# Kernel optimization log

Measured on AMD Instinct MI355X. Metric: run time of the kernel, lower is better.

Reference implementation:

```python
import jax, jax.numpy as jnp
import numpy as np

D = 768; H = 12; T = 8; E = 4; L = 197; B = 4; BT = B * T


def _ln(x, g, b):
    m = x.mean(-1, keepdims=True)
    v = ((x - m) ** 2).mean(-1, keepdims=True)
    return (x - m) / jnp.sqrt(v + 1e-5) * g + b


def _qgelu(x):
    return x * jax.nn.sigmoid(1.702 * x)


def _mha(x, wqkv, bqkv, wo, bo):
    # x: (L, N, D), torch nn.MultiheadAttention semantics (seq-first)
    Lx, N, Dm = x.shape
    hd = Dm // H
    qkv = x @ wqkv.T + bqkv                      # (L, N, 3D)
    q, k, v = jnp.split(qkv, 3, axis=-1)
    sh = lambda t: t.reshape(Lx, N, H, hd).transpose(1, 2, 0, 3)  # (N,H,L,hd)
    q, k, v = sh(q), sh(k), sh(v)
    att = jax.nn.softmax(jnp.einsum('nhld,nhmd->nhlm', q, k) / np.sqrt(hd).astype(np.float32), -1)
    o = jnp.einsum('nhlm,nhmd->nhld', att, v).transpose(2, 0, 1, 3).reshape(Lx, N, Dm)
    return o @ wo.T + bo


def setup_inputs() -> dict:
    key = jax.random.key(0)
    ks = iter(jax.random.split(key, 40))
    s = 0.02
    p = {}
    p['x'] = jax.random.normal(next(ks), (L, BT, D), jnp.float32)
    p['msg_fc_w'] = s * jax.random.normal(next(ks), (D, D)); p['msg_fc_b'] = jnp.zeros((D,))
    p['msg_ln_g'] = jnp.ones((D,)); p['msg_ln_b'] = jnp.zeros((D,))
    p['msg_attn_wqkv'] = s * jax.random.normal(next(ks), (3 * D, D)); p['msg_attn_bqkv'] = jnp.zeros((3 * D,))
    p['msg_attn_wo'] = s * jax.random.normal(next(ks), (D, D)); p['msg_attn_bo'] = jnp.zeros((D,))
    p['attn_wqkv'] = s * jax.random.normal(next(ks), (3 * D, D)); p['attn_bqkv'] = jnp.zeros((3 * D,))
    p['attn_wo'] = s * jax.random.normal(next(ks), (D, D)); p['attn_bo'] = jnp.zeros((D,))
    p['ln1_g'] = jnp.ones((D,)); p['ln1_b'] = jnp.zeros((D,))
    p['ln2_g'] = jnp.ones((D,)); p['ln2_b'] = jnp.zeros((D,))
    p['cfc_w'] = s * jax.random.normal(next(ks), (4 * D, D)); p['cfc_b'] = jnp.zeros((4 * D,))
    p['cproj_w'] = s * jax.random.normal(next(ks), (D, 4 * D)); p['cproj_b'] = jnp.zeros((D,))
    p['eh_w'] = s * jax.random.normal(next(ks), (E, 4 * D, D)); p['eh_b'] = jnp.zeros((E, 4 * D))
    p['et_w'] = s * jax.random.normal(next(ks), (E, D, 4 * D)); p['et_b'] = jnp.zeros((E, D))
    p['r1_w'] = s * jax.random.normal(next(ks), (E + 1, D)); p['r1_b'] = jnp.zeros((E + 1,))
    p['r2_w'] = s * jax.random.normal(next(ks), (E + 1, 4 * D)); p['r2_b'] = jnp.zeros((E + 1,))
    return p


def reference(x, msg_fc_w, msg_fc_b, msg_ln_g, msg_ln_b, msg_attn_wqkv, msg_attn_bqkv,
              msg_attn_wo, msg_attn_bo, attn_wqkv, attn_bqkv, attn_wo, attn_bo,
              ln1_g, ln1_b, ln2_g, ln2_b, cfc_w, cfc_b, cproj_w, cproj_b,
              eh_w, eh_b, et_w, et_b, r1_w, r1_b, r2_w, r2_b):
    l, bt, d = x.shape
    b = bt // T
    x4 = x.reshape(l, b, T, d)
    # message token from CLS (position 0) of each frame
    msg = x4[0] @ msg_fc_w.T + msg_fc_b          # (b, T, d)
    msg = msg.transpose(1, 0, 2)                 # (T, b, d) - attend across frames
    mln = _ln(msg, msg_ln_g, msg_ln_b)
    msg = msg + _mha(mln, msg_attn_wqkv, msg_attn_bqkv, msg_attn_wo, msg_attn_bo)
    msg_r = msg.transpose(1, 0, 2)[None]         # (1, b, T, d)
    xc = jnp.concatenate([x4, msg_r], axis=0).reshape(l + 1, bt, d)
    xc = xc + _mha(_ln(xc, ln1_g, ln1_b), attn_wqkv, attn_bqkv, attn_wo, attn_bo)
    x = xc[:l]
    ln_x = _ln(x, ln2_g, ln2_b)
    # soft-MoE head: shared c_fc is expert 0, then E expert heads
    Wh = jnp.concatenate([cfc_w[None], eh_w], 0)     # (E+1, 4D, D)
    bh = jnp.concatenate([cfc_b[None], eh_b], 0)     # (E+1, 4D)
    heads = jnp.einsum('lbd,efd->lbef', ln_x, Wh) + bh  # (l, bt, E+1, 4D)
    r1 = jax.nn.softmax(ln_x @ r1_w.T + r1_b, -1)       # (l, bt, E+1)
    oh = jnp.einsum('lbe,lbef->lbf', r1, heads)
    oh = _qgelu(oh)
    # soft-MoE tail
    Wt = jnp.concatenate([cproj_w[None], et_w], 0)   # (E+1, D, 4D)
    btl = jnp.concatenate([cproj_b[None], et_b], 0)  # (E+1, D)
    tails = jnp.einsum('lbf,edf->lbed', oh, Wt) + btl  # (l, bt, E+1, D)
    r2 = jax.nn.softmax(oh @ r2_w.T + r2_b, -1)
    out = jnp.einsum('lbe,lbed->lbd', r2, tails)
    return x + out
```

## Files before the change

kernel.cpp:

```cpp
#include <hip/hip_runtime.h>
#include <hip/hip_bf16.h>

typedef __hip_bfloat16 bf16;
typedef __attribute__((ext_vector_type(8))) short short8;
typedef __attribute__((ext_vector_type(4))) float f32x4;

__device__ __forceinline__ float b2f(bf16 v){ return __bfloat162float(v); }
__device__ __forceinline__ unsigned short f2bits(float v){
  bf16 h = __float2bfloat16(v);
  return *reinterpret_cast<unsigned short*>(&h);
}

__device__ __forceinline__ void gload16(const bf16* g, bf16* l){
  __builtin_amdgcn_global_load_lds((const __attribute__((address_space(1))) void*)g,
                                   (__attribute__((address_space(3))) void*)l, 16, 0, 0);
}

__device__ __forceinline__ void ld4(const float* p, float& a,float& b,float& c,float& d){
  float4 v = *reinterpret_cast<const float4*>(p); a=v.x; b=v.y; c=v.z; d=v.w;
}
__device__ __forceinline__ float wave_sum(float v){
  #pragma unroll
  for (int off=32; off>0; off>>=1) v += __shfl_down(v, off);
  return v;
}

__device__ __forceinline__ int xcd_swz(int wg, int nwg){
  int q = nwg >> 3, r = nwg & 7;
  int x = wg & 7, i = wg >> 3;
  return (x < r ? x*(q+1) : r*(q+1) + (x-r)*q) + i;
}

__global__ __launch_bounds__(256) void prep_weights(
    const float* __restrict__ s0, const float* __restrict__ s1,
    const float* __restrict__ s2, const float* __restrict__ s3,
    const float* __restrict__ s4, const float* __restrict__ s5,
    bf16* __restrict__ d0, bf16* __restrict__ d1, bf16* __restrict__ d2,
    bf16* __restrict__ d3, bf16* __restrict__ d4, bf16* __restrict__ d5){
  long i4 = (long)blockIdx.x*256 + threadIdx.x;
  const float* s; bf16* d; long base;
  if      (i4 <  442368){ s=s0; d=d0; base=0; }
  else if (i4 <  589824){ s=s1; d=d1; base=442368; }
  else if (i4 < 1179648){ s=s2; d=d2; base=589824; }
  else if (i4 < 3538944){ s=s3; d=d3; base=1179648; }
  else if (i4 < 4128768){ s=s4; d=d4; base=3538944; }
  else                  { s=s5; d=d5; base=4128768; }
  long j = (i4 - base)*4;
  float4 v = *reinterpret_cast<const float4*>(s + j);
  d[j]   = __float2bfloat16(v.x);
  d[j+1] = __float2bfloat16(v.y);
  d[j+2] = __float2bfloat16(v.z);
  d[j+3] = __float2bfloat16(v.w);
}

__global__ __launch_bounds__(256) void prep_bias(
    const float* __restrict__ cfc_b, const float* __restrict__ eh_b,
    const float* __restrict__ cproj_b, const float* __restrict__ et_b,
    float* __restrict__ bias_h, float* __restrict__ bias_t){
  int i = blockIdx.x*256 + threadIdx.x;
  if (i < 3072)       bias_h[i] = cfc_b[i];
  else if (i < 15360) bias_h[i] = eh_b[i-3072];
  else if (i < 16128) bias_t[i-15360] = cproj_b[i-15360];
  else if (i < 19200) bias_t[i-15360] = et_b[i-16128];
}

__global__ __launch_bounds__(256) void ln_rows(const float* __restrict__ in,
    const float* __restrict__ g, const float* __restrict__ b,
    float* __restrict__ out){
  int row = blockIdx.x;
  const float* x = in + (size_t)row*768;
  float* o = out + (size_t)row*768;
  float s=0.f, s2=0.f;
  for (int d=threadIdx.x; d<768; d+=256){ float v=x[d]; s+=v; s2+=v*v; }
  s = wave_sum(s); s2 = wave_sum(s2);
  __shared__ float red[8];
  __shared__ float stat[2];
  int lane = threadIdx.x & 63, wid = threadIdx.x >> 6;
  if (lane==0){ red[wid]=s; red[4+wid]=s2; }
  __syncthreads();
  if (threadIdx.x==0){
    float S=red[0]+red[1]+red[2]+red[3];
    float S2=red[4]+red[5]+red[6]+red[7];
    float m = S*(1.f/768.f);
    float var = S2*(1.f/768.f) - m*m;
    stat[0]=m; stat[1]=rsqrtf(var + 1e-5f);
  }
  __syncthreads();
  float m=stat[0], inv=stat[1];
  for (int d=threadIdx.x; d<768; d+=256)
    o[d] = (x[d]-m)*inv*g[d] + b[d];
}

__global__ __launch_bounds__(256) void ln_rows_b(const float* __restrict__ in,
    const float* __restrict__ g, const float* __restrict__ b,
    bf16* __restrict__ out){
  int row = blockIdx.x;
  const float* x = in + (size_t)row*768;
  bf16* o = out + (size_t)row*768;
  float s=0.f, s2=0.f;
  for (int d=threadIdx.x; d<768; d+=256){ float v=x[d]; s+=v; s2+=v*v; }
  s = wave_sum(s); s2 = wave_sum(s2);
  __shared__ float red[8];
  __shared__ float stat[2];
  int lane = threadIdx.x & 63, wid = threadIdx.x >> 6;
  if (lane==0){ red[wid]=s; red[4+wid]=s2; }
  __syncthreads();
  if (threadIdx.x==0){
    float S=red[0]+red[1]+red[2]+red[3];
    float S2=red[4]+red[5]+red[6]+red[7];
    float m = S*(1.f/768.f);
    float var = S2*(1.f/768.f) - m*m;
    stat[0]=m; stat[1]=rsqrtf(var + 1e-5f);
  }
  __syncthreads();
  float m=stat[0], inv=stat[1];
  for (int d=threadIdx.x; d<768; d+=256)
    o[d] = __float2bfloat16((x[d]-m)*inv*g[d] + b[d]);
}

template<int K>
__global__ __launch_bounds__(256) void router2(const bf16* __restrict__ X,
    const float* __restrict__ W, const float* __restrict__ bias,
    float* __restrict__ out, int rows){
  int row = blockIdx.x*4 + (threadIdx.x>>6);
  int lane = threadIdx.x & 63;
  if (row >= rows) return;
  const bf16* x = X + (size_t)row*K;
  constexpr int NC = K/64;
  float xa[NC];
  #pragma unroll
  for (int c=0;c<NC;++c) xa[c] = b2f(x[c*64 + lane]);
  float lg[5];
  #pragma unroll
  for (int e=0;e<5;++e){
    const float* w = W + (size_t)e*K;
    float p=0.f;
    #pragma unroll
    for (int c=0;c<NC;++c) p += xa[c]*w[c*64 + lane];
    lg[e] = wave_sum(p);
  }
  if (lane==0){
    float mx=-1e30f;
    #pragma unroll
    for (int e=0;e<5;++e){ lg[e] += bias[e]; mx = fmaxf(mx, lg[e]); }
    float s=0.f;
    #pragma unroll
    for (int e=0;e<5;++e){ lg[e]=expf(lg[e]-mx); s+=lg[e]; }
    float inv=1.f/s;
    #pragma unroll
    for (int e=0;e<5;++e) out[(size_t)row*5+e] = lg[e]*inv;
  }
}

__global__ __launch_bounds__(64) void msg_attn(const float* __restrict__ mqkv,
    float* __restrict__ mattno){
  int bh = blockIdx.x; int b = bh/12, h = bh%12;
  __shared__ float qs[8][64], ks[8][64], vs[8][64], sc[8][8];
  int lane = threadIdx.x;
  for (int i=lane; i<512; i+=64){
    int t=i>>6, d=i&63;
    size_t base = ((size_t)(b*8+t))*2304 + h*64 + d;
    qs[t][d]=mqkv[base]; ks[t][d]=mqkv[base+768]; vs[t][d]=mqkv[base+1536];
  }
  __syncthreads();
  { int t=lane>>3, m=lane&7; float a=0.f;
    #pragma unroll
    for (int d=0;d<64;++d) a += qs[t][d]*ks[m][d];
    sc[t][m] = a*0.125f; }
  __syncthreads();
  if (lane<8){
    int t=lane; float mx=-1e30f;
    #pragma unroll
    for (int m=0;m<8;++m) mx=fmaxf(mx, sc[t][m]);
    float s=0.f;
    #pragma unroll
    for (int m=0;m<8;++m){ float e=expf(sc[t][m]-mx); sc[t][m]=e; s+=e; }
    float inv=1.f/s;
    #pragma unroll
    for (int m=0;m<8;++m) sc[t][m]*=inv;
  }
  __syncthreads();
  { int t=lane>>3, d0=(lane&7)*8;
    for (int dd=0; dd<8; ++dd){
      int d=d0+dd; float a=0.f;
      #pragma unroll
      for (int m=0;m<8;++m) a += sc[t][m]*vs[m][d];
      mattno[((size_t)(b*8+t))*768 + h*64 + d] = a;
    } }
}

__global__ __launch_bounds__(256) void attn_mfma(const bf16* __restrict__ qkv,
    bf16* __restrict__ attno){
  constexpr int KP = 232;
  __shared__ __align__(16) unsigned short Ks[208*72];
  __shared__ __align__(16) unsigned short Vt[64*KP];
  __shared__ __align__(16) unsigned short Ps[4*16*KP];

  int tid = threadIdx.x;
  int bh = blockIdx.x; int bb = bh/12, h = bh%12;
  int l0 = blockIdx.y*64;
  int wv = tid>>6, ln = tid&63, quad = ln>>4, mrow = ln&15;

  for (int i=tid; i<1584; i+=256){
    int m=i>>3, dc=(i&7)<<3;
    const uint4 kv = *reinterpret_cast<const uint4*>(qkv + ((size_t)(m*32+bb))*2304 + 768 + h*64 + dc);
    *reinterpret_cast<uint4*>(Ks + m*72 + dc) = kv;
    const uint4 vv = *reinterpret_cast<const uint4*>(qkv + ((size_t)(m*32+bb))*2304 + 1536 + h*64 + dc);
    unsigned int w[4] = {vv.x, vv.y, vv.z, vv.w};
    #pragma unroll
    for (int j=0;j<4;++j){
      Vt[(dc+2*j  )*KP + m] = (unsigned short)(w[j] & 0xffff);
      Vt[(dc+2*j+1)*KP + m] = (unsigned short)(w[j] >> 16);
    }
  }
  for (int i=tid; i<10*72; i+=256) Ks[198*72 + i] = 0;
  for (int i=tid; i<64*34; i+=256){ int d=i/34, c=198+(i%34); Vt[d*KP+c] = 0; }
  { unsigned int* pz = reinterpret_cast<unsigned int*>(Ps);
    for (int i=tid; i<4*16*KP/2; i+=256) pz[i] = 0; }

  int ql = l0 + wv*16 + mrow;
  short8 aq[2] = { {0,0,0,0,0,0,0,0}, {0,0,0,0,0,0,0,0} };
  if (ql < 198){
    aq[0] = *reinterpret_cast<const short8*>(qkv + ((size_t)(ql*32+bb))*2304 + h*64 + quad*8);
    aq[1] = *reinterpret_cast<const short8*>(qkv + ((size_t)(ql*32+bb))*2304 + h*64 + 32 + quad*8);
  }
  __syncthreads();

  f32x4 sc[13];
  const f32x4 zero = {0.f,0.f,0.f,0.f};
  #pragma unroll
  for (int t=0;t<13;++t){
    const short8 bk0 = *reinterpret_cast<const short8*>(Ks + (t*16+mrow)*72 + quad*8);
    const short8 bk1 = *reinterpret_cast<const short8*>(Ks + (t*16+mrow)*72 + 32 + quad*8);
    f32x4 a = zero;
    a = __builtin_amdgcn_mfma_f32_16x16x32_bf16(aq[0], bk0, a, 0,0,0);
    a = __builtin_amdgcn_mfma_f32_16x16x32_bf16(aq[1], bk1, a, 0,0,0);
    sc[t] = a * 0.125f;
  }
  if (192 + mrow >= 198) sc[12] = (f32x4){-1e30f,-1e30f,-1e30f,-1e30f};

  float inv[4];
  #pragma unroll
  for (int r=0;r<4;++r){
    float m = -1e30f;
    #pragma unroll
    for (int t=0;t<13;++t) m = fmaxf(m, sc[t][r]);
    #pragma unroll
    for (int msk=1; msk<16; msk<<=1) m = fmaxf(m, __shfl_xor(m, msk));
    float s = 0.f;
    #pragma unroll
    for (int t=0;t<13;++t){ float e = __expf(sc[t][r]-m); sc[t][r]=e; s+=e; }
    #pragma unroll
    for (int msk=1; msk<16; msk<<=1) s += __shfl_xor(s, msk);
    inv[r] = 1.f/s;
  }

  #pragma unroll
  for (int t=0;t<13;++t)
    #pragma unroll
    for (int r=0;r<4;++r)
      Ps[(wv*16 + quad*4+r)*KP + t*16+mrow] = f2bits(sc[t][r]);
  __syncthreads();

  f32x4 o[4] = {zero,zero,zero,zero};
  #pragma unroll
  for (int kc=0;kc<7;++kc){
    const short8 ap = *reinterpret_cast<const short8*>(Ps + (wv*16+mrow)*KP + kc*32 + quad*8);
    #pragma unroll
    for (int nt=0;nt<4;++nt){
      const short8 bv = *reinterpret_cast<const short8*>(Vt + (nt*16+mrow)*KP + kc*32 + quad*8);
      o[nt] = __builtin_amdgcn_mfma_f32_16x16x32_bf16(ap, bv, o[nt], 0,0,0);
    }
  }
  #pragma unroll
  for (int r=0;r<4;++r){
    int l = l0 + wv*16 + quad*4 + r;
    if (l >= 198) continue;
    #pragma unroll
    for (int nt=0;nt<4;++nt){
      int d = nt*16 + mrow;
      attno[((size_t)(l*32+bb))*768 + h*64 + d] = __float2bfloat16(o[nt][r]*inv[r]);
    }
  }
}

__global__ __launch_bounds__(256) void gemm_nt(const float* __restrict__ A,
    const float* __restrict__ B, const float* __restrict__ bias,
    const float* res, float* C,
    int M, int N, int K){
  __shared__ __align__(16) float As[16][68];
  __shared__ __align__(16) float Bs[16][68];
  int tid=threadIdx.x, tx=tid&15, ty=tid>>4;
  int row0=blockIdx.y*64, col0=blockIdx.x*64;
  int lrow=tid>>2, lk4=(tid&3)*4;
  float acc[4][4]={};
  for (int kb=0; kb<K; kb+=16){
    int gr = row0 + lrow;
    if (gr < M){
      float a0,a1,a2,a3; ld4(A + (size_t)gr*K + kb + lk4, a0,a1,a2,a3);
      As[lk4][lrow]=a0; As[lk4+1][lrow]=a1; As[lk4+2][lrow]=a2; As[lk4+3][lrow]=a3;
    } else {
      As[lk4][lrow]=0.f; As[lk4+1][lrow]=0.f; As[lk4+2][lrow]=0.f; As[lk4+3][lrow]=0.f;
    }
    { float c0,c1,c2,c3; ld4(B + (size_t)(col0+lrow)*K + kb + lk4, c0,c1,c2,c3);
      Bs[lk4][lrow]=c0; Bs[lk4+1][lrow]=c1; Bs[lk4+2][lrow]=c2; Bs[lk4+3][lrow]=c3; }
    __syncthreads();
    #pragma unroll
    for (int kk=0;kk<16;++kk){
      float4 a4 = *reinterpret_cast<const float4*>(&As[kk][ty*4]);
      float4 b4 = *reinterpret_cast<const float4*>(&Bs[kk][tx*4]);
      float av[4]={a4.x,a4.y,a4.z,a4.w};
      float bw[4]={b4.x,b4.y,b4.z,b4.w};
      #pragma unroll
      for (int u=0;u<4;++u)
        #pragma unroll
        for (int v=0;v<4;++v) acc[u][v] += av[u]*bw[v];
    }
    __syncthreads();
  }
  #pragma unroll
  for (int u=0;u<4;++u){
    int gi = row0 + ty*4 + u;
    if (gi >= M) continue;
    #pragma unroll
    for (int v=0;v<4;++v){
      int gj = col0 + tx*4 + v;
      float r = res ? res[(size_t)gi*N+gj] : 0.f;
      float bb = bias ? bias[gj] : 0.f;
      C[(size_t)gi*N+gj] = r + acc[u][v] + bb;
    }
  }
}

template<int MODE>
__global__ __launch_bounds__(256,3) void gemm_mfma(
    const bf16* __restrict__ A, const bf16* __restrict__ B,
    const float* __restrict__ bias,
    const float* res, float* __restrict__ outf,
    bf16* __restrict__ outb, int M, int N, int K)
{
  __shared__ __align__(16) bf16 As0[4096];
  __shared__ __align__(16) bf16 As1[4096];
  __shared__ __align__(16) bf16 Bs0[4096];
  __shared__ __align__(16) bf16 Bs1[4096];

  int tid=threadIdx.x, wv=tid>>6, ln=tid&63;
  int quad=ln>>4, mrow=ln&15;
  int row0=blockIdx.y*128, col0=blockIdx.x*128;
  int wr=wv>>1, wc=wv&1;

  int c0 = wv*64 + ln;
  int r0 = c0>>2, cc=(c0&3)*8;

  int aoff[4], boff[4];
  #pragma unroll
  for (int i=0;i<4;++i){
    aoff[i] = (wr*64 + i*16 + mrow)*32 + quad*8;
    boff[i] = (wc*64 + i*16 + mrow)*32 + quad*8;
  }

  f32x4 acc[4][4];
  const f32x4 zero = {0.f,0.f,0.f,0.f};
  #pragma unroll
  for (int i=0;i<4;++i)
    #pragma unroll
    for (int j=0;j<4;++j) acc[i][j]=zero;

  const bf16* Ab = A + (size_t)(row0+r0)*K + cc;
  const bf16* Bb = B + (size_t)(col0+r0)*K + cc;
  for (int kb=0; kb<K; kb+=64){
    gload16(Ab + kb,                As0 + wv*512);
    gload16(Ab + (size_t)64*K + kb, As0 + 2048 + wv*512);
    gload16(Bb + kb,                Bs0 + wv*512);
    gload16(Bb + (size_t)64*K + kb, Bs0 + 2048 + wv*512);
    gload16(Ab + kb + 32,                As1 + wv*512);
    gload16(Ab + (size_t)64*K + kb + 32, As1 + 2048 + wv*512);
    gload16(Bb + kb + 32,                Bs1 + wv*512);
    gload16(Bb + (size_t)64*K + kb + 32, Bs1 + 2048 + wv*512);
    __syncthreads();
    short8 af[4], bfr[4];
    #pragma unroll
    for (int i=0;i<4;++i) af[i]  = *reinterpret_cast<const short8*>(As0 + aoff[i]);
    #pragma unroll
    for (int j=0;j<4;++j) bfr[j] = *reinterpret_cast<const short8*>(Bs0 + boff[j]);
    #pragma unroll
    for (int i=0;i<4;++i)
      #pragma unroll
      for (int j=0;j<4;++j)
        acc[i][j] = __builtin_amdgcn_mfma_f32_16x16x32_bf16(af[i], bfr[j], acc[i][j], 0, 0, 0);
    #pragma unroll
    for (int i=0;i<4;++i) af[i]  = *reinterpret_cast<const short8*>(As1 + aoff[i]);
    #pragma unroll
    for (int j=0;j<4;++j) bfr[j] = *reinterpret_cast<const short8*>(Bs1 + boff[j]);
    #pragma unroll
    for (int i=0;i<4;++i)
      #pragma unroll
      for (int j=0;j<4;++j)
        acc[i][j] = __builtin_amdgcn_mfma_f32_16x16x32_bf16(af[i], bfr[j], acc[i][j], 0, 0, 0);
    __syncthreads();
  }

  #pragma unroll
  for (int i=0;i<4;++i){
    #pragma unroll
    for (int r=0;r<4;++r){
      int gi = row0 + wr*64 + i*16 + quad*4 + r;
      if (gi >= M) continue;
      #pragma unroll
      for (int j=0;j<4;++j){
        int gj = col0 + wc*64 + j*16 + mrow;
        if (MODE==0) outb[(size_t)gi*N+gj] = __float2bfloat16(acc[i][j][r] + bias[gj]);
        else         outf[(size_t)gi*N+gj] = acc[i][j][r] + bias[gj] + res[(size_t)gi*N+gj];
      }
    }
  }
}

template<int MODE>
__global__ __launch_bounds__(256,2) void gemm_moe3(
    const bf16* __restrict__ A, const bf16* __restrict__ B,
    const float* __restrict__ bias, const float* __restrict__ rmat,
    const float* __restrict__ res, float* __restrict__ outf,
    bf16* __restrict__ outb, int M, int N, int K)
{
  __shared__ __align__(16) bf16 As[64*32];
  __shared__ __align__(16) bf16 Bs[5*128*32];

  int tid=threadIdx.x, wv=tid>>6, ln=tid&63;
  int quad=ln>>4, mrow=ln&15;

  int gy = (M + 63) >> 6;
  int lin = xcd_swz(blockIdx.x, gridDim.x);
  int bx = lin / gy, by = lin % gy;
  int row0 = by*64, col0 = bx*128;

  int r0 = tid>>2, cc=(tid&3)*8;

  int aoff[4], boff[2];
  #pragma unroll
  for (int i=0;i<4;++i) aoff[i] = (i*16 + mrow)*32 + quad*8;
  #pragma unroll
  for (int j=0;j<2;++j) boff[j] = (wv*32 + j*16 + mrow)*32 + quad*8;

  const f32x4 zero = {0.f,0.f,0.f,0.f};
  f32x4 acc[5][4][2];
  #pragma unroll
  for (int e=0;e<5;++e)
    #pragma unroll
    for (int i=0;i<4;++i)
      #pragma unroll
      for (int j=0;j<2;++j) acc[e][i][j]=zero;

  const bf16* Ab = A + (size_t)(row0+r0)*K + cc;
  const bf16* Bb = B + (size_t)(col0+r0)*K + cc;

  for (int kb=0; kb<K; kb+=32){
    gload16(Ab + kb, As + wv*512);
    #pragma unroll
    for (int e=0;e<5;++e){
      const bf16* Be = Bb + (size_t)e*N*K + kb;
      gload16(Be,                Bs + e*4096 + wv*512);
      gload16(Be + (size_t)64*K, Bs + e*4096 + 2048 + wv*512);
    }
    __syncthreads();
    short8 af[4];
    #pragma unroll
    for (int i=0;i<4;++i) af[i] = *reinterpret_cast<const short8*>(As + aoff[i]);
    #pragma unroll
    for (int e=0;e<5;++e){
      const short8 b0 = *reinterpret_cast<const short8*>(Bs + e*4096 + boff[0]);
      const short8 b1 = *reinterpret_cast<const short8*>(Bs + e*4096 + boff[1]);
      #pragma unroll
      for (int i=0;i<4;++i){
        acc[e][i][0] = __builtin_amdgcn_mfma_f32_16x16x32_bf16(af[i], b0, acc[e][i][0], 0, 0, 0);
        acc[e][i][1] = __builtin_amdgcn_mfma_f32_16x16x32_bf16(af[i], b1, acc[e][i][1], 0, 0, 0);
      }
    }
    __syncthreads();
  }

  float bv[5][2];
  #pragma unroll
  for (int e=0;e<5;++e)
    #pragma unroll
    for (int j=0;j<2;++j)
      bv[e][j] = bias[(size_t)e*N + col0 + wv*32 + j*16 + mrow];

  #pragma unroll
  for (int i=0;i<4;++i){
    #pragma unroll
    for (int r=0;r<4;++r){
      int gi = row0 + i*16 + quad*4 + r;
      if (gi >= M) continue;
      const float* rp = rmat + (size_t)gi*5;
      float w0=rp[0], w1=rp[1], w2=rp[2], w3=rp[3], w4=rp[4];
      #pragma unroll
      for (int j=0;j<2;++j){
        int gj = col0 + wv*32 + j*16 + mrow;
        float v = w0*(acc[0][i][j][r]+bv[0][j])
                + w1*(acc[1][i][j][r]+bv[1][j])
                + w2*(acc[2][i][j][r]+bv[2][j])
                + w3*(acc[3][i][j][r]+bv[3][j])
                + w4*(acc[4][i][j][r]+bv[4][j]);
        if (MODE==0){
          float q = v / (1.f + __expf(-1.702f*v));
          outb[(size_t)gi*N+gj] = __float2bfloat16(q);
        } else {
          outf[(size_t)gi*N+gj] = v + res[(size_t)gi*N+gj];
        }
      }
    }
  }
}

extern "C" void kernel_launch(void* const* d_in, const int* in_sizes, int n_in,
                              void* d_out, int out_size, void* d_ws, size_t ws_size,
                              hipStream_t stream) {
  const float* x         = (const float*)d_in[0];
  const float* msg_fc_w  = (const float*)d_in[1];
  const float* msg_fc_b  = (const float*)d_in[2];
  const float* msg_ln_g  = (const float*)d_in[3];
  const float* msg_ln_b  = (const float*)d_in[4];
  const float* msg_wqkv  = (const float*)d_in[5];
  const float* msg_bqkv  = (const float*)d_in[6];
  const float* msg_wo    = (const float*)d_in[7];
  const float* msg_bo    = (const float*)d_in[8];
  const float* attn_wqkv = (const float*)d_in[9];
  const float* attn_bqkv = (const float*)d_in[10];
  const float* attn_wo   = (const float*)d_in[11];
  const float* attn_bo   = (const float*)d_in[12];
  const float* ln1_g     = (const float*)d_in[13];
  const float* ln1_b     = (const float*)d_in[14];
  const float* ln2_g     = (const float*)d_in[15];
  const float* ln2_b     = (const float*)d_in[16];
  const float* cfc_w     = (const float*)d_in[17];
  const float* cfc_b     = (const float*)d_in[18];
  const float* cproj_w   = (const float*)d_in[19];
  const float* cproj_b   = (const float*)d_in[20];
  const float* eh_w      = (const float*)d_in[21];
  const float* eh_b      = (const float*)d_in[22];
  const float* et_w      = (const float*)d_in[23];
  const float* et_b      = (const float*)d_in[24];
  const float* r1_w      = (const float*)d_in[25];
  const float* r1_b      = (const float*)d_in[26];
  const float* r2_w      = (const float*)d_in[27];
  const float* r2_b      = (const float*)d_in[28];
  float* out = (float*)d_out;

  float* ws     = (float*)d_ws;
  float* xc     = ws;
  float* bigA   = xc + 4866048;
  bf16*  qkv_b  = (bf16*)bigA;
  bf16*  oh_b   = (bf16*)bigA;
  float* lnbf   = bigA + 9830400;
  bf16*  lnb_b  = (bf16*)lnbf;
  float* attnof = lnbf + 2457600;
  bf16*  attno_b= (bf16*)attnof;
  float* wqf    = attnof + 2457600;
  bf16*  wq_b   = (bf16*)wqf;
  float* wof    = wqf + 884736;
  bf16*  wo_b   = (bf16*)wof;
  float* whf    = wof + 294912;
  bf16*  wh_b   = (bf16*)whf;
  float* wtf    = whf + 5898240;
  bf16*  wt_b   = (bf16*)wtf;
  float* bias_h = wtf + 5898240;
  float* bias_t = bias_h + 15360;
  float* r1b    = bias_t + 3840;
  float* r2b    = r1b + 32000;
  float* msg    = r2b + 32000;
  float* mln    = msg + 24576;
  float* mqkv   = mln + 24576;
  float* matt   = mqkv + 73728;

  prep_weights<<<dim3(6488064/256), 256, 0, stream>>>(
      attn_wqkv, attn_wo, cfc_w, eh_w, cproj_w, et_w,
      wq_b, wo_b, wh_b, wh_b + 2359296, wt_b, wt_b + 2359296);
  prep_bias<<<dim3(75), 256, 0, stream>>>(cfc_b, eh_b, cproj_b, et_b, bias_h, bias_t);

  hipMemcpyAsync(xc, x, (size_t)4841472*sizeof(float), hipMemcpyDeviceToDevice, stream);
  gemm_nt<<<dim3(12,1), 256, 0, stream>>>(x, msg_fc_w, msg_fc_b, nullptr, msg, 32, 768, 768);
  ln_rows<<<dim3(32), 256, 0, stream>>>(msg, msg_ln_g, msg_ln_b, mln);
  gemm_nt<<<dim3(36,1), 256, 0, stream>>>(mln, msg_wqkv, msg_bqkv, nullptr, mqkv, 32, 2304, 768);
  msg_attn<<<dim3(48), 64, 0, stream>>>(mqkv, matt);
  gemm_nt<<<dim3(12,1), 256, 0, stream>>>(matt, msg_wo, msg_bo, msg, xc + (size_t)6304*768, 32, 768, 768);
  ln_rows_b<<<dim3(6336), 256, 0, stream>>>(xc, ln1_g, ln1_b, lnb_b);
  gemm_mfma<0><<<dim3(18,50), 256, 0, stream>>>(lnb_b, wq_b, attn_bqkv, nullptr, nullptr, qkv_b, 6336, 2304, 768);
  attn_mfma<<<dim3(384,4), 256, 0, stream>>>(qkv_b, attno_b);
  gemm_mfma<1><<<dim3(6,50), 256, 0, stream>>>(attno_b, wo_b, attn_bo, xc, xc, nullptr, 6336, 768, 768);
  ln_rows_b<<<dim3(6304), 256, 0, stream>>>(xc, ln2_g, ln2_b, lnb_b);
  router2<768><<<dim3(1576), 256, 0, stream>>>(lnb_b, r1_w, r1_b, r1b, 6304);
  gemm_moe3<0><<<dim3(24*99), 256, 0, stream>>>(lnb_b, wh_b, bias_h, r1b, nullptr, nullptr, oh_b, 6304, 3072, 768);
  router2<3072><<<dim3(1576), 256, 0, stream>>>(oh_b, r2_w, r2_b, r2b, 6304);
  gemm_moe3<1><<<dim3(6*99), 256, 0, stream>>>(oh_b, wt_b, bias_t, r2b, xc, out, nullptr, 6304, 768, 3072);
}
```

Measured before the change: 1.030 ms.

## Double-buffer MoE GEMM with 64x96 tiles, 2x2 wave layout and grouped rasterization

Rewrites the fused soft-MoE GEMM to double-buffer the A and B shared-memory tiles, so the next K-slab's global-to-LDS loads overlap the current slab's MFMAs and one barrier per iteration is removed. The block tile changes from 64x128 to 64x96, with a 2x2 wave arrangement replacing the 1x4 layout. Block indices are remapped into column groups to improve L2 reuse of the weights. The cost is doubled LDS use (about 68KB per block), which may limit occupancy, plus more blocks and redundant clamped loads for the unused B rows.

```diff
diff --git a/kernel.cpp b/kernel.cpp
--- a/kernel.cpp
+++ b/kernel.cpp
@@ -417,86 +417,106 @@
 }
 
 template<int MODE>
-__global__ __launch_bounds__(256,2) void gemm_moe3(
+__global__ __launch_bounds__(256,2) void gemm_moe5(
     const bf16* __restrict__ A, const bf16* __restrict__ B,
     const float* __restrict__ bias, const float* __restrict__ rmat,
     const float* __restrict__ res, float* __restrict__ outf,
-    bf16* __restrict__ outb, int M, int N, int K)
+    bf16* __restrict__ outb, int M, int N, int K, int NR, int G)
 {
-  __shared__ __align__(16) bf16 As[64*32];
-  __shared__ __align__(16) bf16 Bs[5*128*32];
+  __shared__ __align__(16) bf16 As[2][2048];
+  __shared__ __align__(16) bf16 Bs[2][16384];
 
   int tid=threadIdx.x, wv=tid>>6, ln=tid&63;
   int quad=ln>>4, mrow=ln&15;
-
-  int gy = (M + 63) >> 6;
+  int wr=wv>>1, wc=wv&1;
+
   int lin = xcd_swz(blockIdx.x, gridDim.x);
-  int bx = lin / gy, by = lin % gy;
-  int row0 = by*64, col0 = bx*128;
+  int gsz = G*NR;
+  int grp = lin/gsz, rem = lin - grp*gsz;
+  int by = rem / G, bx = grp*G + rem % G;
+  int row0 = by*64, col0 = bx*96;
 
   int r0 = tid>>2, cc=(tid&3)*8;
 
-  int aoff[4], boff[2];
-  #pragma unroll
-  for (int i=0;i<4;++i) aoff[i] = (i*16 + mrow)*32 + quad*8;
-  #pragma unroll
-  for (int j=0;j<2;++j) boff[j] = (wv*32 + j*16 + mrow)*32 + quad*8;
+  int aoff[2], boff[3];
+  #pragma unroll
+  for (int i=0;i<2;++i) aoff[i] = (wr*32 + i*16 + mrow)*32 + quad*8;
+  #pragma unroll
+  for (int j=0;j<3;++j) boff[j] = (wc*48 + j*16 + mrow)*32 + quad*8;
 
   const f32x4 zero = {0.f,0.f,0.f,0.f};
-  f32x4 acc[5][4][2];
+  f32x4 acc[5][2][3];
   #pragma unroll
   for (int e=0;e<5;++e)
     #pragma unroll
-    for (int i=0;i<4;++i)
+    for (int i=0;i<2;++i)
       #pragma unroll
-      for (int j=0;j<2;++j) acc[e][i][j]=zero;
+      for (int j=0;j<3;++j) acc[e][i][j]=zero;
 
   const bf16* Ab = A + (size_t)(row0+r0)*K + cc;
-  const bf16* Bb = B + (size_t)(col0+r0)*K + cc;
-
-  for (int kb=0; kb<K; kb+=32){
-    gload16(Ab + kb, As + wv*512);
+  const bf16* Bb = B + (size_t)(col0 + (ln>>2))*K + (ln&3)*8;
+
+  size_t brow[8];
+  #pragma unroll
+  for (int k_=0;k_<8;++k_){
+    int u  = wv*8 + k_;
+    int uu = (u < 30) ? u : 29;
+    int e_ = uu/6, rb_ = uu - e_*6;
+    brow[k_] = ((size_t)e_*N + rb_*16)*K;
+  }
+  int ubase = wv*8*512;
+
+#define MOE5_STAGE(buf, kb) { \
+    gload16(Ab + (kb), &As[buf][wv*512]); \
+    _Pragma("unroll") \
+    for (int k_=0;k_<8;++k_) \
+      gload16(Bb + brow[k_] + (kb), &Bs[buf][ubase + k_*512]); \
+  }
+
+  int nk = K >> 5;
+  MOE5_STAGE(0, 0);
+  __syncthreads();
+
+  int cur = 0;
+  for (int t=0; t<nk; ++t){
+    if (t+1 < nk){ MOE5_STAGE(cur^1, (t+1)*32); }
+    short8 af0 = *reinterpret_cast<const short8*>(&As[cur][aoff[0]]);
+    short8 af1 = *reinterpret_cast<const short8*>(&As[cur][aoff[1]]);
     #pragma unroll
     for (int e=0;e<5;++e){
-      const bf16* Be = Bb + (size_t)e*N*K + kb;
-      gload16(Be,                Bs + e*4096 + wv*512);
-      gload16(Be + (size_t)64*K, Bs + e*4096 + 2048 + wv*512);
+      const short8 b0 = *reinterpret_cast<const short8*>(&Bs[cur][e*3072 + boff[0]]);
+      const short8 b1 = *reinterpret_cast<const short8*>(&Bs[cur][e*3072 + boff[1]]);
+      const short8 b2 = *reinterpret_cast<const short8*>(&Bs[cur][e*3072 + boff[2]]);
+      acc[e][0][0] = __builtin_amdgcn_mfma_f32_16x16x32_bf16(af0, b0, acc[e][0][0], 0,0,0);
+      acc[e][0][1] = __builtin_amdgcn_mfma_f32_16x16x32_bf16(af0, b1, acc[e][0][1], 0,0,0);
+      acc[e][0][2] = __builtin_amdgcn_mfma_f32_16x16x32_bf16(af0, b2, acc[e][0][2], 0,0,0);
+      acc[e][1][0] = __builtin_amdgcn_mfma_f32_16x16x32_bf16(af1, b0, acc[e][1][0], 0,0,0);
+      acc[e][1][1] = __builtin_amdgcn_mfma_f32_16x16x32_bf16(af1, b1, acc[e][1][1], 0,0,0);
+      acc[e][1][2] = __builtin_amdgcn_mfma_f32_16x16x32_bf16(af1, b2, acc[e][1][2], 0,0,0);
     }
     __syncthreads();
-    short8 af[4];
-    #pragma unroll
-    for (int i=0;i<4;++i) af[i] = *reinterpret_cast<const short8*>(As + aoff[i]);
-    #pragma unroll
-    for (int e=0;e<5;++e){
-      const short8 b0 = *reinterpret_cast<const short8*>(Bs + e*4096 + boff[0]);
-      const short8 b1 = *reinterpret_cast<const short8*>(Bs + e*4096 + boff[1]);
-      #pragma unroll
-      for (int i=0;i<4;++i){
-        acc[e][i][0] = __builtin_amdgcn_mfma_f32_16x16x32_bf16(af[i], b0, acc[e][i][0], 0, 0, 0);
-        acc[e][i][1] = __builtin_amdgcn_mfma_f32_16x16x32_bf16(af[i], b1, acc[e][i][1], 0, 0, 0);
-      }
-    }
-    __syncthreads();
-  }
-
-  float bv[5][2];
+    cur ^= 1;
+  }
+#undef MOE5_STAGE
+
+  float bv[5][3];
   #pragma unroll
   for (int e=0;e<5;++e)
     #pragma unroll
-    for (int j=0;j<2;++j)
-      bv[e][j] = bias[(size_t)e*N + col0 + wv*32 + j*16 + mrow];
-
-  #pragma unroll
-  for (int i=0;i<4;++i){
+    for (int j=0;j<3;++j)
+      bv[e][j] = bias[(size_t)e*N + col0 + wc*48 + j*16 + mrow];
+
+  #pragma unroll
+  for (int i=0;i<2;++i){
     #pragma unroll
     for (int r=0;r<4;++r){
-      int gi = row0 + i*16 + quad*4 + r;
+      int gi = row0 + wr*32 + i*16 + quad*4 + r;
       if (gi >= M) continue;
       const float* rp = rmat + (size_t)gi*5;
       float w0=rp[0], w1=rp[1], w2=rp[2], w3=rp[3], w4=rp[4];
       #pragma unroll
-      for (int j=0;j<2;++j){
-        int gj = col0 + wv*32 + j*16 + mrow;
+      for (int j=0;j<3;++j){
+        int gj = col0 + wc*48 + j*16 + mrow;
         float v = w0*(acc[0][i][j][r]+bv[0][j])
                 + w1*(acc[1][i][j][r]+bv[1][j])
                 + w2*(acc[2][i][j][r]+bv[2][j])
@@ -590,7 +610,7 @@
   gemm_mfma<1><<<dim3(6,50), 256, 0, stream>>>(attno_b, wo_b, attn_bo, xc, xc, nullptr, 6336, 768, 768);
   ln_rows_b<<<dim3(6304), 256, 0, stream>>>(xc, ln2_g, ln2_b, lnb_b);
   router2<768><<<dim3(1576), 256, 0, stream>>>(lnb_b, r1_w, r1_b, r1b, 6304);
-  gemm_moe3<0><<<dim3(24*99), 256, 0, stream>>>(lnb_b, wh_b, bias_h, r1b, nullptr, nullptr, oh_b, 6304, 3072, 768);
+  gemm_moe5<0><<<dim3(3168), 256, 0, stream>>>(lnb_b, wh_b, bias_h, r1b, nullptr, nullptr, oh_b, 6304, 3072, 768, 99, 4);
   router2<3072><<<dim3(1576), 256, 0, stream>>>(oh_b, r2_w, r2_b, r2b, 6304);
-  gemm_moe3<1><<<dim3(6*99), 256, 0, stream>>>(oh_b, wt_b, bias_t, r2b, xc, out, nullptr, 6304, 768, 3072);
-}
+  gemm_moe5<1><<<dim3(792), 256, 0, stream>>>(oh_b, wt_b, bias_t, r2b, xc, out, nullptr, 6304, 768, 3072, 99, 1);
+}
```

After: 1.005 ms. 2.4% less time.
